# Kernel tuning notes

Hardware: AMD Instinct MI355X
Metric: run time of the kernel (lower is better)

Reference implementation:

```python
import jax, jax.numpy as jnp
import numpy as np

N = 6144       # nodes
E = 12288      # edges (~2N for a sparse simplicial complex)
NF = 32        # node features
EF = 16        # edge features
NH = [32, 32]  # node_hidden
EH = [16, 16]  # edge_hidden
EPS = 1e-5


def setup_inputs() -> dict:
    key = jax.random.key(0)
    ks = jax.random.split(key, 24)
    s = 0.1  # weight init scale
    inp = {}
    inp["X_n"] = jax.random.normal(ks[0], (N, NF), jnp.float32)
    inp["X_e"] = jax.random.normal(ks[1], (E, EF), jnp.float32)
    # normalized adjacency-like operator (non-negative, row mass ~1)
    inp["A_tilde"] = jax.random.uniform(ks[2], (N, N), jnp.float32) * (1.0 / N)
    # normalized Hodge-1 Laplacian-like operator
    inp["L1_tilde"] = jax.random.normal(ks[3], (E, E), jnp.float32) * (1.0 / np.sqrt(E))
    # incidence-like operator
    inp["B1"] = jax.random.normal(ks[4], (N, E), jnp.float32) * (1.0 / np.sqrt(E))
    # GNN linear layers: weight [out, in] (torch convention)
    inp["gnn_W0"] = jax.random.normal(ks[5], (NH[0], NF), jnp.float32) * s
    inp["gnn_b0"] = jnp.zeros((NH[0],), jnp.float32)
    inp["gnn_W1"] = jax.random.normal(ks[6], (NH[1], NH[0]), jnp.float32) * s
    inp["gnn_b1"] = jnp.zeros((NH[1],), jnp.float32)
    # HoSC layer 0: theta in=EF out=EH[0], BN params
    inp["th_W0"] = jax.random.normal(ks[7], (EH[0], EF), jnp.float32) * s
    inp["th_b0"] = jnp.zeros((EH[0],), jnp.float32)
    inp["bn_g0"] = jnp.ones((EH[0],), jnp.float32)
    inp["bn_b0"] = jnp.zeros((EH[0],), jnp.float32)
    # HoSC layer 1: input collapses to 1 channel (max keepdim)
    inp["th_W1"] = jax.random.normal(ks[8], (EH[1], 1), jnp.float32) * s
    inp["th_b1"] = jnp.zeros((EH[1],), jnp.float32)
    inp["bn_g1"] = jnp.ones((EH[1],), jnp.float32)
    inp["bn_b1"] = jnp.zeros((EH[1],), jnp.float32)
    # head: fc1 in = NH[-1] + len(EH) = 34, out = 2N; fc2 out = 1
    inp["fc1_W"] = jax.random.normal(ks[9], (2 * N, NH[-1] + len(EH)), jnp.float32) * s
    inp["fc1_b"] = jnp.zeros((2 * N,), jnp.float32)
    inp["fc2_W"] = jax.random.normal(ks[10], (1, 2 * N), jnp.float32) * s
    inp["fc2_b"] = jnp.zeros((1,), jnp.float32)
    return inp


def _gnn_layer(A, H, W, b):
    # H <- relu((A @ H) @ W^T + b)
    return jax.nn.relu(jnp.matmul(jnp.matmul(A, H), W.T) + b)


def _hosc_layer(Z, L1, W, b, g, beta):
    Zt = jnp.matmul(Z, W.T) + b            # theta
    Zc = jnp.matmul(L1, Zt)                # Laplacian conv
    m = jnp.mean(Zc, axis=0)               # BatchNorm1d (training-mode batch stats)
    v = jnp.var(Zc, axis=0)
    Zp = jax.nn.relu(g * (Zc - m) * jax.lax.rsqrt(v + EPS) + beta)
    return jnp.max(Zp, axis=1, keepdims=True)  # [E, 1]


def reference(X_n, X_e, A_tilde, L1_tilde, B1,
              gnn_W0, gnn_b0, gnn_W1, gnn_b1,
              th_W0, th_b0, bn_g0, bn_b0,
              th_W1, th_b1, bn_g1, bn_b1,
              fc1_W, fc1_b, fc2_W, fc2_b):
    # GNN over nodes
    H = _gnn_layer(A_tilde, X_n, gnn_W0, gnn_b0)
    H_n = _gnn_layer(A_tilde, H, gnn_W1, gnn_b1)      # [N, NH[-1]]
    # HoSC over edges
    Z0 = _hosc_layer(X_e, L1_tilde, th_W0, th_b0, bn_g0, bn_b0)  # [E, 1]
    Z1 = _hosc_layer(Z0, L1_tilde, th_W1, th_b1, bn_g1, bn_b1)   # [E, 1]
    Z_cat = jnp.concatenate([Z0, Z1], axis=1)         # [E, 2]
    H_e = jnp.matmul(B1, Z_cat)                       # [N, 2]
    # head
    Hcat = jnp.concatenate([H_n, H_e], axis=1)        # [N, 34]
    f = jax.nn.relu(jnp.matmul(Hcat, fc1_W.T) + fc1_b)
    f = jnp.matmul(f, fc2_W.T) + fc2_b                # [N, 1]
    return jax.nn.sigmoid(f).squeeze(-1)              # [N]
```

## Files before the change

kernel.cpp:

```cpp
#include <hip/hip_runtime.h>
#include <hip/hip_cooperative_groups.h>
#include <math.h>

namespace cg = cooperative_groups;

#define NND 6144
#define NED 12288
#define GRID 1024
static constexpr float EPS_BN = 1e-5f;

#define HN_OFF    0
#define HE_OFF    196608
#define ST_OFF    208896
#define Y_OFF     208960
#define T0_OFF    405568
#define T1_OFF    602176
#define Z0_OFF    798784
#define Z1_OFF    811072
#define U_OFF     823360
#define S_OFF     835648
#define PP_OFF    847936

typedef float floatx4 __attribute__((ext_vector_type(4)));

__device__ __forceinline__ float4 ntload4(const float* p) {
  floatx4 v = __builtin_nontemporal_load(reinterpret_cast<const floatx4*>(p));
  return make_float4(v.x, v.y, v.z, v.w);
}
__device__ __forceinline__ float4 ld4(const float* p) {
  return *reinterpret_cast<const float4*>(p);
}
__device__ __forceinline__ void gll16(const float* g, float* l) {
  __builtin_amdgcn_global_load_lds(
      (const __attribute__((address_space(1))) unsigned int*)g,
      (__attribute__((address_space(3))) unsigned int*)l, 16, 0, 0);
}

struct Params {
  const float *X_n, *X_e, *A, *L1, *B1;
  const float *gW0, *gb0, *gW1, *gb1;
  const float *tW0, *tb0, *bng0, *bnb0;
  const float *tW1, *tb1, *bng1, *bnb1;
  const float *fc1W, *fc1b, *fc2W, *fc2b;
  float *ws;
  float *out;
};

template<int PHASE>
__global__ __launch_bounds__(256, 4) void pipeline(Params p) {
  __shared__ float lds[10240];
  float* sst = &lds[10176];
  float* red = &lds[10208];

  const int tid  = threadIdx.x;
  const int lane = tid & 63;
  const int w    = tid >> 6;
  const int blk  = blockIdx.x;
  const int gtid = blk * 256 + tid;
  constexpr bool ALL = (PHASE == 0);

  float* Hn = p.ws + HN_OFF;
  float* he = p.ws + HE_OFF;
  float* st = p.ws + ST_OFF;
  float* Y  = p.ws + Y_OFF;
  float* T0 = p.ws + T0_OFF;
  float* T1 = p.ws + T1_OFF;
  float* Z0 = p.ws + Z0_OFF;
  float* Z1 = p.ws + Z1_OFF;
  float* u  = p.ws + U_OFF;
  float* s  = p.ws + S_OFF;
  float* pp = p.ws + PP_OFF;

  auto gemm32 = [&](const float* bias, float* outp) {
    const int rg = w >> 1, cg_ = w & 1;
    const int r0 = blk * 6;
    const int c0 = cg_ * 16;
    float acc[3][16];
    #pragma unroll
    for (int r = 0; r < 3; ++r)
      #pragma unroll
      for (int c = 0; c < 16; ++c) acc[r][c] = 0.f;

    for (int kb = 0; kb < NND; kb += 256) {
      #pragma unroll
      for (int i = 0; i < 8; ++i) {
        const int yr = w * 8 + i;
        gll16(Y + (size_t)yr * NND + kb + lane * 4, &lds[yr * 256]);
      }
      #pragma unroll
      for (int i = 0; i < 2; ++i) {
        const int ar = w * 2 + i;
        if (ar < 6)
          gll16(p.A + (size_t)(r0 + ar) * NND + kb + lane * 4, &lds[8192 + ar * 256]);
      }
      __syncthreads();
      float4 av[3];
      #pragma unroll
      for (int r = 0; r < 3; ++r)
        av[r] = ld4(&lds[8192 + (rg * 3 + r) * 256 + lane * 4]);
      #pragma unroll
      for (int c = 0; c < 16; ++c) {
        const float4 y = ld4(&lds[(c0 + c) * 256 + lane * 4]);
        #pragma unroll
        for (int r = 0; r < 3; ++r) {
          acc[r][c] = fmaf(av[r].x, y.x, acc[r][c]);
          acc[r][c] = fmaf(av[r].y, y.y, acc[r][c]);
          acc[r][c] = fmaf(av[r].z, y.z, acc[r][c]);
          acc[r][c] = fmaf(av[r].w, y.w, acc[r][c]);
        }
      }
      __syncthreads();
    }
    #pragma unroll
    for (int r = 0; r < 3; ++r) {
      float wv[16];
      #pragma unroll
      for (int c = 0; c < 16; ++c) {
        float t = acc[r][c] + __shfl_xor(acc[r][c], 32, 64);
        wv[c] = t + __shfl_xor(t, 16, 64);
      }
      #pragma unroll
      for (int b = 3; b >= 0; --b) {
        const int m = 1 << b;
        const bool hi = (lane & m) != 0;
        #pragma unroll
        for (int i = 0; i < (1 << b); ++i) {
          float x = wv[i], yv = wv[i + (1 << b)];
          float send = hi ? x : yv;
          float recv = __shfl_xor(send, m, 64);
          wv[i] = (hi ? yv : x) + recv;
        }
      }
      if (lane < 16) {
        float v = fmaxf(wv[0] + bias[c0 + lane], 0.f);
        outp[(size_t)(r0 + rg * 3 + r) * 32 + c0 + lane] = v;
      }
    }
  };

  if constexpr (ALL || PHASE == 1) {
    if (blk == 0 && tid < 64) st[tid] = 0.f;
    if (gtid < NND) {
      const int m = gtid;
      float x[32];
      #pragma unroll
      for (int k = 0; k < 32; k += 4) {
        float4 v = ld4(p.X_n + (size_t)m * 32 + k);
        x[k] = v.x; x[k+1] = v.y; x[k+2] = v.z; x[k+3] = v.w;
      }
      #pragma unroll
      for (int oc = 0; oc < 32; ++oc) {
        float acc = 0.f;
        #pragma unroll
        for (int k = 0; k < 32; ++k) acc = fmaf(x[k], p.gW0[oc * 32 + k], acc);
        Y[(size_t)oc * NND + m] = acc;
      }
    } else if (gtid < NND + NED) {
      const int e = gtid - NND;
      float x[16];
      #pragma unroll
      for (int k = 0; k < 16; k += 4) {
        float4 v = ld4(p.X_e + (size_t)e * 16 + k);
        x[k] = v.x; x[k+1] = v.y; x[k+2] = v.z; x[k+3] = v.w;
      }
      #pragma unroll
      for (int oc = 0; oc < 16; ++oc) {
        float acc = p.tb0[oc];
        #pragma unroll
        for (int k = 0; k < 16; ++k) acc = fmaf(x[k], p.tW0[oc * 16 + k], acc);
        T1[(size_t)oc * NED + e] = acc;
      }
    }
  }
  if constexpr (ALL) cg::this_grid().sync();

  if constexpr (ALL || PHASE == 2) gemm32(p.gb0, T0);
  if constexpr (ALL) cg::this_grid().sync();

  if constexpr (ALL || PHASE == 3) {
    if (gtid < NND) {
      const int m = gtid;
      float x[32];
      #pragma unroll
      for (int k = 0; k < 32; k += 4) {
        float4 v = ld4(T0 + (size_t)m * 32 + k);
        x[k] = v.x; x[k+1] = v.y; x[k+2] = v.z; x[k+3] = v.w;
      }
      #pragma unroll
      for (int oc = 0; oc < 32; ++oc) {
        float acc = 0.f;
        #pragma unroll
        for (int k = 0; k < 32; ++k) acc = fmaf(x[k], p.gW1[oc * 32 + k], acc);
        Y[(size_t)oc * NND + m] = acc;
      }
    }
  }
  if constexpr (ALL) cg::this_grid().sync();

  if constexpr (ALL || PHASE == 4) gemm32(p.gb1, Hn);
  if constexpr (ALL) cg::this_grid().sync();

  if constexpr (ALL || PHASE == 5) {
    const int r0 = blk * 12;
    float acc[3][16];
    #pragma unroll
    for (int r = 0; r < 3; ++r)
      #pragma unroll
      for (int c = 0; c < 16; ++c) acc[r][c] = 0.f;

    for (int kb = 0; kb < NED; kb += 256) {
      #pragma unroll
      for (int i = 0; i < 4; ++i) {
        const int yr = w * 4 + i;
        gll16(T1 + (size_t)yr * NED + kb + lane * 4, &lds[yr * 256]);
      }
      #pragma unroll
      for (int i = 0; i < 3; ++i) {
        const int ar = w * 3 + i;
        gll16(p.L1 + (size_t)(r0 + ar) * NED + kb + lane * 4, &lds[4096 + ar * 256]);
      }
      __syncthreads();
      float4 av[3];
      #pragma unroll
      for (int r = 0; r < 3; ++r)
        av[r] = ld4(&lds[4096 + (w * 3 + r) * 256 + lane * 4]);
      #pragma unroll
      for (int c = 0; c < 16; ++c) {
        const float4 y = ld4(&lds[c * 256 + lane * 4]);
        #pragma unroll
        for (int r = 0; r < 3; ++r) {
          acc[r][c] = fmaf(av[r].x, y.x, acc[r][c]);
          acc[r][c] = fmaf(av[r].y, y.y, acc[r][c]);
          acc[r][c] = fmaf(av[r].z, y.z, acc[r][c]);
          acc[r][c] = fmaf(av[r].w, y.w, acc[r][c]);
        }
      }
      __syncthreads();
    }
    float stS = 0.f, stQ = 0.f;
    #pragma unroll
    for (int r = 0; r < 3; ++r) {
      float wv[16];
      #pragma unroll
      for (int c = 0; c < 16; ++c) {
        float t = acc[r][c] + __shfl_xor(acc[r][c], 32, 64);
        wv[c] = t + __shfl_xor(t, 16, 64);
      }
      #pragma unroll
      for (int b = 3; b >= 0; --b) {
        const int m = 1 << b;
        const bool hi = (lane & m) != 0;
        #pragma unroll
        for (int i = 0; i < (1 << b); ++i) {
          float x = wv[i], yv = wv[i + (1 << b)];
          float send = hi ? x : yv;
          float recv = __shfl_xor(send, m, 64);
          wv[i] = (hi ? yv : x) + recv;
        }
      }
      if (lane < 16) {
        const float v = wv[0];
        T0[(size_t)(r0 + w * 3 + r) * 16 + lane] = v;
        stS += v; stQ += v * v;
      }
    }
    if (tid < 32) sst[tid] = 0.f;
    __syncthreads();
    if (lane < 16) {
      atomicAdd(&sst[lane], stS);
      atomicAdd(&sst[16 + lane], stQ);
    }
    __syncthreads();
    if (tid < 32) atomicAdd(st + tid, sst[tid]);
  }
  if constexpr (ALL) cg::this_grid().sync();

  if constexpr (ALL || PHASE == 6) {
    if (gtid < NED) {
      const int e = gtid;
      const float invE = 1.f / (float)NED;
      float best = -3.4e38f;
      #pragma unroll
      for (int c = 0; c < 16; ++c) {
        float m = st[c] * invE;
        float var = st[16 + c] * invE - m * m;
        float sc = p.bng0[c] * rsqrtf(var + EPS_BN);
        float sh = p.bnb0[c] - m * sc;
        best = fmaxf(best, fmaf(T0[(size_t)e * 16 + c], sc, sh));
      }
      Z0[e] = fmaxf(best, 0.f);
    }
  }
  if constexpr (ALL) cg::this_grid().sync();

  if constexpr (ALL || PHASE == 7) {
    const int rb = GRID - 1 - blk;
    const int r0 = rb * 12 + w * 3;
    const float* mp[3];
    #pragma unroll
    for (int r = 0; r < 3; ++r) mp[r] = p.L1 + (size_t)(r0 + r) * NED;
    float ua[3] = {0,0,0}, sa[3] = {0,0,0};
    float4 a[3], an[3];
    #pragma unroll
    for (int r = 0; r < 3; ++r) a[r] = ntload4(mp[r] + lane * 4);
    float4 z = ld4(Z0 + lane * 4), zn;
    for (int kb = 0; kb < NED; kb += 256) {
      const int k = kb + lane * 4;
      const bool more = (kb + 256) < NED;
      if (more) {
        #pragma unroll
        for (int r = 0; r < 3; ++r) an[r] = ntload4(mp[r] + k + 256);
        zn = ld4(Z0 + k + 256);
      }
      #pragma unroll
      for (int r = 0; r < 3; ++r) {
        ua[r] += a[r].x*z.x + a[r].y*z.y + a[r].z*z.z + a[r].w*z.w;
        sa[r] += a[r].x + a[r].y + a[r].z + a[r].w;
      }
      if (more) {
        #pragma unroll
        for (int r = 0; r < 3; ++r) a[r] = an[r];
        z = zn;
      }
    }
    #pragma unroll
    for (int r = 0; r < 3; ++r)
      #pragma unroll
      for (int m = 1; m < 64; m <<= 1) {
        ua[r] += __shfl_xor(ua[r], m, 64);
        sa[r] += __shfl_xor(sa[r], m, 64);
      }
    if (lane == 0) {
      float s1 = 0.f, s2 = 0.f, s3 = 0.f, s4 = 0.f, s5 = 0.f;
      #pragma unroll
      for (int r = 0; r < 3; ++r) {
        u[r0 + r] = ua[r]; s[r0 + r] = sa[r];
        s1 += ua[r]; s2 += sa[r];
        s3 += ua[r] * ua[r]; s4 += sa[r] * sa[r]; s5 += ua[r] * sa[r];
      }
      red[w * 5 + 0] = s1; red[w * 5 + 1] = s2; red[w * 5 + 2] = s3;
      red[w * 5 + 3] = s4; red[w * 5 + 4] = s5;
    }
    __syncthreads();
    if (tid < 5)
      atomicAdd(st + 32 + tid, red[tid] + red[5 + tid] + red[10 + tid] + red[15 + tid]);
  }
  if constexpr (ALL) cg::this_grid().sync();

  if constexpr (ALL || PHASE == 8) {
    if (gtid < NED) {
      const int e = gtid;
      const float invE = 1.f / (float)NED;
      const float Su = st[32], Ss = st[33], Suu = st[34], Sss = st[35], Sus = st[36];
      const float uu = u[e], ssv = s[e];
      float best = -3.4e38f;
      #pragma unroll
      for (int c = 0; c < 16; ++c) {
        const float wc = p.tW1[c], bc = p.tb1[c];
        const float mean = (wc * Su + bc * Ss) * invE;
        const float ex2 = (wc * wc * Suu + 2.f * wc * bc * Sus + bc * bc * Sss) * invE;
        const float var = ex2 - mean * mean;
        const float sc = p.bng1[c] * rsqrtf(var + EPS_BN);
        const float sh = p.bnb1[c] - mean * sc;
        best = fmaxf(best, fmaf(wc * uu + bc * ssv, sc, sh));
      }
      Z1[e] = fmaxf(best, 0.f);
    }
  }
  if constexpr (ALL) cg::this_grid().sync();

  if constexpr (ALL || PHASE == 9) {
    const int r0 = blk * 12 + w * 3;
    if (r0 < NND) {
      const float* mp[3];
      #pragma unroll
      for (int r = 0; r < 3; ++r) mp[r] = p.B1 + (size_t)(r0 + r) * NED;
      float uu[3] = {0,0,0}, vv[3] = {0,0,0};
      float4 a[3], an[3];
      #pragma unroll
      for (int r = 0; r < 3; ++r) a[r] = ntload4(mp[r] + lane * 4);
      float4 z = ld4(Z0 + lane * 4), y = ld4(Z1 + lane * 4), zn, yn;
      for (int kb = 0; kb < NED; kb += 256) {
        const int k = kb + lane * 4;
        const bool more = (kb + 256) < NED;
        if (more) {
          #pragma unroll
          for (int r = 0; r < 3; ++r) an[r] = ntload4(mp[r] + k + 256);
          zn = ld4(Z0 + k + 256); yn = ld4(Z1 + k + 256);
        }
        #pragma unroll
        for (int r = 0; r < 3; ++r) {
          uu[r] += a[r].x*z.x + a[r].y*z.y + a[r].z*z.z + a[r].w*z.w;
          vv[r] += a[r].x*y.x + a[r].y*y.y + a[r].z*y.z + a[r].w*y.w;
        }
        if (more) {
          #pragma unroll
          for (int r = 0; r < 3; ++r) a[r] = an[r];
          z = zn; y = yn;
        }
      }
      #pragma unroll
      for (int r = 0; r < 3; ++r)
        #pragma unroll
        for (int m = 1; m < 64; m <<= 1) {
          uu[r] += __shfl_xor(uu[r], m, 64);
          vv[r] += __shfl_xor(vv[r], m, 64);
        }
      if (lane == 0) {
        #pragma unroll
        for (int r = 0; r < 3; ++r) {
          he[(r0 + r) * 2]     = uu[r];
          he[(r0 + r) * 2 + 1] = vv[r];
        }
      }
    }
  }
  if constexpr (ALL) cg::this_grid().sync();

  if constexpr (ALL || PHASE == 10) {
    const int nb = blk & 7, jb = blk >> 3;
    int n[3];
    float h[3][34];
    float acc[3] = {0.f, 0.f, 0.f};
    #pragma unroll
    for (int i = 0; i < 3; ++i) {
      n[i] = nb * 768 + i * 256 + tid;
      #pragma unroll
      for (int k = 0; k < 32; k += 4) {
        float4 v = ld4(Hn + (size_t)n[i] * 32 + k);
        h[i][k] = v.x; h[i][k+1] = v.y; h[i][k+2] = v.z; h[i][k+3] = v.w;
      }
      float2 e2 = *reinterpret_cast<const float2*>(he + n[i] * 2);
      h[i][32] = e2.x; h[i][33] = e2.y;
    }
    const int j0 = jb * 96;
    for (int j = j0; j < j0 + 96; ++j) {
      const float* wp = p.fc1W + (size_t)j * 34;
      const float bj = p.fc1b[j], vj = p.fc2W[j];
      float s0 = bj, s1 = bj, s2 = bj;
      #pragma unroll
      for (int k = 0; k < 34; ++k) {
        const float wk = wp[k];
        s0 = fmaf(h[0][k], wk, s0);
        s1 = fmaf(h[1][k], wk, s1);
        s2 = fmaf(h[2][k], wk, s2);
      }
      acc[0] += fmaxf(s0, 0.f) * vj;
      acc[1] += fmaxf(s1, 0.f) * vj;
      acc[2] += fmaxf(s2, 0.f) * vj;
    }
    #pragma unroll
    for (int i = 0; i < 3; ++i) pp[(size_t)jb * NND + n[i]] = acc[i];
  }
  if constexpr (ALL) cg::this_grid().sync();

  if constexpr (ALL || PHASE == 11) {
    if (gtid < NND) {
      float acc = 0.f;
      for (int j = 0; j < 128; ++j) acc += pp[(size_t)j * NND + gtid];
      p.out[gtid] = 1.f / (1.f + expf(-(acc + p.fc2b[0])));
    }
  }
}

extern "C" void kernel_launch(void* const* d_in, const int* in_sizes, int n_in,
                              void* d_out, int out_size, void* d_ws, size_t ws_size,
                              hipStream_t stream) {
  Params p;
  p.X_n  = (const float*)d_in[0];
  p.X_e  = (const float*)d_in[1];
  p.A    = (const float*)d_in[2];
  p.L1   = (const float*)d_in[3];
  p.B1   = (const float*)d_in[4];
  p.gW0  = (const float*)d_in[5];
  p.gb0  = (const float*)d_in[6];
  p.gW1  = (const float*)d_in[7];
  p.gb1  = (const float*)d_in[8];
  p.tW0  = (const float*)d_in[9];
  p.tb0  = (const float*)d_in[10];
  p.bng0 = (const float*)d_in[11];
  p.bnb0 = (const float*)d_in[12];
  p.tW1  = (const float*)d_in[13];
  p.tb1  = (const float*)d_in[14];
  p.bng1 = (const float*)d_in[15];
  p.bnb1 = (const float*)d_in[16];
  p.fc1W = (const float*)d_in[17];
  p.fc1b = (const float*)d_in[18];
  p.fc2W = (const float*)d_in[19];
  p.fc2b = (const float*)d_in[20];
  p.ws   = (float*)d_ws;
  p.out  = (float*)d_out;

  int maxBlk = 0;
  hipError_t oe = hipOccupancyMaxActiveBlocksPerMultiprocessor(
      &maxBlk, pipeline<0>, 256, 0);
  bool coop_ok = (oe == hipSuccess) && (maxBlk >= 4);

  if (coop_ok) {
    void* kargs[] = { &p };
    hipError_t le = hipLaunchCooperativeKernel(
        (const void*)&pipeline<0>, dim3(GRID), dim3(256), kargs, 0, stream);
    if (le == hipSuccess) return;
  }

  pipeline<1><<<GRID, 256, 0, stream>>>(p);
  pipeline<2><<<GRID, 256, 0, stream>>>(p);
  pipeline<3><<<GRID, 256, 0, stream>>>(p);
  pipeline<4><<<GRID, 256, 0, stream>>>(p);
  pipeline<5><<<GRID, 256, 0, stream>>>(p);
  pipeline<6><<<GRID, 256, 0, stream>>>(p);
  pipeline<7><<<GRID, 256, 0, stream>>>(p);
  pipeline<8><<<GRID, 256, 0, stream>>>(p);
  pipeline<9><<<GRID, 256, 0, stream>>>(p);
  pipeline<10><<<GRID, 256, 0, stream>>>(p);
  pipeline<11><<<GRID, 256, 0, stream>>>(p);
}
```

Baseline: 578.3 us.

## Double-buffer the second Laplacian GEMM with register prefetch of L1 rows

Phase 5 (L1 times the staged T1 tile) now loads the L1 rows straight into registers and prefetches the next chunk while computing the current one. The T1 tile is double-buffered in LDS through async global-to-LDS loads, and waits use explicit vmcnt counts plus raw s_barrier. This is meant to hide global memory latency behind the FMA loop and drop one barrier per iteration. In exchange it uses more registers and relies on hand-counted vmcnt values, and the launch bounds are rewritten as a waves-per-EU attribute.

```diff
diff --git a/kernel.cpp b/kernel.cpp
--- a/kernel.cpp
+++ b/kernel.cpp
@@ -47,7 +47,9 @@
 };
 
 template<int PHASE>
-__global__ __launch_bounds__(256, 4) void pipeline(Params p) {
+__global__ __launch_bounds__(256)
+__attribute__((amdgpu_waves_per_eu(4, 4)))
+void pipeline(Params p) {
   __shared__ float lds[10240];
   float* sst = &lds[10176];
   float* red = &lds[10208];
@@ -202,41 +204,64 @@
 
   if constexpr (ALL || PHASE == 5) {
     const int r0 = blk * 12;
+    const float* mp[3];
+    #pragma unroll
+    for (int r = 0; r < 3; ++r) mp[r] = p.L1 + (size_t)(r0 + w * 3 + r) * NED;
+
     float acc[3][16];
     #pragma unroll
     for (int r = 0; r < 3; ++r)
       #pragma unroll
       for (int c = 0; c < 16; ++c) acc[r][c] = 0.f;
 
-    for (int kb = 0; kb < NED; kb += 256) {
+    auto stageZt = [&](int kb, int b) {
       #pragma unroll
       for (int i = 0; i < 4; ++i) {
         const int yr = w * 4 + i;
-        gll16(T1 + (size_t)yr * NED + kb + lane * 4, &lds[yr * 256]);
-      }
-      #pragma unroll
-      for (int i = 0; i < 3; ++i) {
-        const int ar = w * 3 + i;
-        gll16(p.L1 + (size_t)(r0 + ar) * NED + kb + lane * 4, &lds[4096 + ar * 256]);
-      }
-      __syncthreads();
-      float4 av[3];
-      #pragma unroll
-      for (int r = 0; r < 3; ++r)
-        av[r] = ld4(&lds[4096 + (w * 3 + r) * 256 + lane * 4]);
+        gll16(T1 + (size_t)yr * NED + kb + lane * 4, &lds[b * 4096 + yr * 256]);
+      }
+    };
+    float4 aC[3], aN[3];
+    auto issueA = [&](int kb, float4* d) {
+      #pragma unroll
+      for (int r = 0; r < 3; ++r) d[r] = ld4(mp[r] + kb + lane * 4);
+    };
+
+    issueA(0, aC);
+    stageZt(0, 0);
+    asm volatile("s_waitcnt vmcnt(0)" ::: "memory");
+    __builtin_amdgcn_sched_barrier(0);
+    __builtin_amdgcn_s_barrier();
+
+    constexpr int NCH = NED / 256;
+    for (int i = 0; i < NCH; ++i) {
+      const int pb = i & 1;
+      const bool more = (i + 1) < NCH;
+      if (more) {
+        issueA((i + 1) * 256, aN);
+        stageZt((i + 1) * 256, pb ^ 1);
+        asm volatile("s_waitcnt vmcnt(7)" ::: "memory");
+      } else {
+        asm volatile("s_waitcnt vmcnt(0)" ::: "memory");
+      }
+      __builtin_amdgcn_sched_barrier(0);
+      __builtin_amdgcn_s_barrier();
+      __builtin_amdgcn_sched_barrier(0);
       #pragma unroll
       for (int c = 0; c < 16; ++c) {
-        const float4 y = ld4(&lds[c * 256 + lane * 4]);
+        const float4 y = ld4(&lds[pb * 4096 + c * 256 + lane * 4]);
         #pragma unroll
         for (int r = 0; r < 3; ++r) {
-          acc[r][c] = fmaf(av[r].x, y.x, acc[r][c]);
-          acc[r][c] = fmaf(av[r].y, y.y, acc[r][c]);
-          acc[r][c] = fmaf(av[r].z, y.z, acc[r][c]);
-          acc[r][c] = fmaf(av[r].w, y.w, acc[r][c]);
-        }
-      }
-      __syncthreads();
-    }
+          acc[r][c] = fmaf(aC[r].x, y.x, acc[r][c]);
+          acc[r][c] = fmaf(aC[r].y, y.y, acc[r][c]);
+          acc[r][c] = fmaf(aC[r].z, y.z, acc[r][c]);
+          acc[r][c] = fmaf(aC[r].w, y.w, acc[r][c]);
+        }
+      }
+      if (more) { aC[0] = aN[0]; aC[1] = aN[1]; aC[2] = aN[2]; }
+      __builtin_amdgcn_s_barrier();
+    }
+
     float stS = 0.f, stQ = 0.f;
     #pragma unroll
     for (int r = 0; r < 3; ++r) {
```

After: 592.7 us. 2.5% more time.

## Merge independent GNN and HoSC phases to cut grid barriers

Applied to the files above, without the earlier changes.

Interleaves the node-GNN stages with the edge-HoSC stages, which do not depend on each other, so each grid-synchronised phase does both a GNN step and a Laplacian step. This drops the phase count from eleven to eight, and with it the number of cooperative grid syncs or fallback launches. The head is re-tiled to one node per thread over 768 blocks with 384 hidden units each, and the final reduction now sums 32 partials instead of 128. Launch bounds change to a waves_per_eu attribute. Merged phases become longer and less balanced, and the head leaves some blocks idle.

```diff
diff --git a/kernel.cpp b/kernel.cpp
--- a/kernel.cpp
+++ b/kernel.cpp
@@ -14,12 +14,13 @@
 #define ST_OFF    208896
 #define Y_OFF     208960
 #define T0_OFF    405568
-#define T1_OFF    602176
-#define Z0_OFF    798784
-#define Z1_OFF    811072
-#define U_OFF     823360
-#define S_OFF     835648
-#define PP_OFF    847936
+#define ZT_OFF    602176
+#define ZC_OFF    798784
+#define Z0_OFF    995392
+#define Z1_OFF    1007680
+#define U_OFF     1019968
+#define S_OFF     1032256
+#define PP_OFF    1044544
 
 typedef float floatx4 __attribute__((ext_vector_type(4)));
 
@@ -47,7 +48,9 @@
 };
 
 template<int PHASE>
-__global__ __launch_bounds__(256, 4) void pipeline(Params p) {
+__global__ __launch_bounds__(256)
+__attribute__((amdgpu_waves_per_eu(4, 4)))
+void pipeline(Params p) {
   __shared__ float lds[10240];
   float* sst = &lds[10176];
   float* red = &lds[10208];
@@ -64,7 +67,8 @@
   float* st = p.ws + ST_OFF;
   float* Y  = p.ws + Y_OFF;
   float* T0 = p.ws + T0_OFF;
-  float* T1 = p.ws + T1_OFF;
+  float* ZT = p.ws + ZT_OFF;
+  float* ZC = p.ws + ZC_OFF;
   float* Z0 = p.ws + Z0_OFF;
   float* Z1 = p.ws + Z1_OFF;
   float* u  = p.ws + U_OFF;
@@ -168,39 +172,15 @@
         float acc = p.tb0[oc];
         #pragma unroll
         for (int k = 0; k < 16; ++k) acc = fmaf(x[k], p.tW0[oc * 16 + k], acc);
-        T1[(size_t)oc * NED + e] = acc;
-      }
-    }
-  }
-  if constexpr (ALL) cg::this_grid().sync();
-
-  if constexpr (ALL || PHASE == 2) gemm32(p.gb0, T0);
-  if constexpr (ALL) cg::this_grid().sync();
-
-  if constexpr (ALL || PHASE == 3) {
-    if (gtid < NND) {
-      const int m = gtid;
-      float x[32];
-      #pragma unroll
-      for (int k = 0; k < 32; k += 4) {
-        float4 v = ld4(T0 + (size_t)m * 32 + k);
-        x[k] = v.x; x[k+1] = v.y; x[k+2] = v.z; x[k+3] = v.w;
-      }
-      #pragma unroll
-      for (int oc = 0; oc < 32; ++oc) {
-        float acc = 0.f;
-        #pragma unroll
-        for (int k = 0; k < 32; ++k) acc = fmaf(x[k], p.gW1[oc * 32 + k], acc);
-        Y[(size_t)oc * NND + m] = acc;
-      }
-    }
-  }
-  if constexpr (ALL) cg::this_grid().sync();
-
-  if constexpr (ALL || PHASE == 4) gemm32(p.gb1, Hn);
-  if constexpr (ALL) cg::this_grid().sync();
-
-  if constexpr (ALL || PHASE == 5) {
+        ZT[(size_t)oc * NED + e] = acc;
+      }
+    }
+  }
+  if constexpr (ALL) cg::this_grid().sync();
+
+  if constexpr (ALL || PHASE == 2) {
+    gemm32(p.gb0, T0);
+
     const int r0 = blk * 12;
     float acc[3][16];
     #pragma unroll
@@ -212,7 +192,7 @@
       #pragma unroll
       for (int i = 0; i < 4; ++i) {
         const int yr = w * 4 + i;
-        gll16(T1 + (size_t)yr * NED + kb + lane * 4, &lds[yr * 256]);
+        gll16(ZT + (size_t)yr * NED + kb + lane * 4, &lds[yr * 256]);
       }
       #pragma unroll
       for (int i = 0; i < 3; ++i) {
@@ -260,7 +240,7 @@
       }
       if (lane < 16) {
         const float v = wv[0];
-        T0[(size_t)(r0 + w * 3 + r) * 16 + lane] = v;
+        ZC[(size_t)(r0 + w * 3 + r) * 16 + lane] = v;
         stS += v; stQ += v * v;
       }
     }
@@ -275,9 +255,24 @@
   }
   if constexpr (ALL) cg::this_grid().sync();
 
-  if constexpr (ALL || PHASE == 6) {
-    if (gtid < NED) {
-      const int e = gtid;
+  if constexpr (ALL || PHASE == 3) {
+    if (gtid < NND) {
+      const int m = gtid;
+      float x[32];
+      #pragma unroll
+      for (int k = 0; k < 32; k += 4) {
+        float4 v = ld4(T0 + (size_t)m * 32 + k);
+        x[k] = v.x; x[k+1] = v.y; x[k+2] = v.z; x[k+3] = v.w;
+      }
+      #pragma unroll
+      for (int oc = 0; oc < 32; ++oc) {
+        float acc = 0.f;
+        #pragma unroll
+        for (int k = 0; k < 32; ++k) acc = fmaf(x[k], p.gW1[oc * 32 + k], acc);
+        Y[(size_t)oc * NND + m] = acc;
+      }
+    } else if (gtid < NND + NED) {
+      const int e = gtid - NND;
       const float invE = 1.f / (float)NED;
       float best = -3.4e38f;
       #pragma unroll
@@ -286,14 +281,16 @@
         float var = st[16 + c] * invE - m * m;
         float sc = p.bng0[c] * rsqrtf(var + EPS_BN);
         float sh = p.bnb0[c] - m * sc;
-        best = fmaxf(best, fmaf(T0[(size_t)e * 16 + c], sc, sh));
+        best = fmaxf(best, fmaf(ZC[(size_t)e * 16 + c], sc, sh));
       }
       Z0[e] = fmaxf(best, 0.f);
     }
   }
   if constexpr (ALL) cg::this_grid().sync();
 
-  if constexpr (ALL || PHASE == 7) {
+  if constexpr (ALL || PHASE == 4) {
+    gemm32(p.gb1, Hn);
+
     const int rb = GRID - 1 - blk;
     const int r0 = rb * 12 + w * 3;
     const float* mp[3];
@@ -347,7 +344,7 @@
   }
   if constexpr (ALL) cg::this_grid().sync();
 
-  if constexpr (ALL || PHASE == 8) {
+  if constexpr (ALL || PHASE == 5) {
     if (gtid < NED) {
       const int e = gtid;
       const float invE = 1.f / (float)NED;
@@ -369,7 +366,7 @@
   }
   if constexpr (ALL) cg::this_grid().sync();
 
-  if constexpr (ALL || PHASE == 9) {
+  if constexpr (ALL || PHASE == 6) {
     const int r0 = blk * 12 + w * 3;
     if (r0 < NND) {
       const float* mp[3];
@@ -417,47 +414,37 @@
   }
   if constexpr (ALL) cg::this_grid().sync();
 
-  if constexpr (ALL || PHASE == 10) {
-    const int nb = blk & 7, jb = blk >> 3;
-    int n[3];
-    float h[3][34];
-    float acc[3] = {0.f, 0.f, 0.f};
-    #pragma unroll
-    for (int i = 0; i < 3; ++i) {
-      n[i] = nb * 768 + i * 256 + tid;
+  if constexpr (ALL || PHASE == 7) {
+    if (blk < 768) {
+      const int nb = blk % 24, jb = blk / 24;
+      const int n = nb * 256 + tid;
+      float h[34];
       #pragma unroll
       for (int k = 0; k < 32; k += 4) {
-        float4 v = ld4(Hn + (size_t)n[i] * 32 + k);
-        h[i][k] = v.x; h[i][k+1] = v.y; h[i][k+2] = v.z; h[i][k+3] = v.w;
-      }
-      float2 e2 = *reinterpret_cast<const float2*>(he + n[i] * 2);
-      h[i][32] = e2.x; h[i][33] = e2.y;
-    }
-    const int j0 = jb * 96;
-    for (int j = j0; j < j0 + 96; ++j) {
-      const float* wp = p.fc1W + (size_t)j * 34;
-      const float bj = p.fc1b[j], vj = p.fc2W[j];
-      float s0 = bj, s1 = bj, s2 = bj;
-      #pragma unroll
-      for (int k = 0; k < 34; ++k) {
-        const float wk = wp[k];
-        s0 = fmaf(h[0][k], wk, s0);
-        s1 = fmaf(h[1][k], wk, s1);
-        s2 = fmaf(h[2][k], wk, s2);
-      }
-      acc[0] += fmaxf(s0, 0.f) * vj;
-      acc[1] += fmaxf(s1, 0.f) * vj;
-      acc[2] += fmaxf(s2, 0.f) * vj;
-    }
-    #pragma unroll
-    for (int i = 0; i < 3; ++i) pp[(size_t)jb * NND + n[i]] = acc[i];
-  }
-  if constexpr (ALL) cg::this_grid().sync();
-
-  if constexpr (ALL || PHASE == 11) {
+        float4 v = ld4(Hn + (size_t)n * 32 + k);
+        h[k] = v.x; h[k+1] = v.y; h[k+2] = v.z; h[k+3] = v.w;
+      }
+      float2 e2 = *reinterpret_cast<const float2*>(he + n * 2);
+      h[32] = e2.x; h[33] = e2.y;
+      float acc = 0.f;
+      const int j0 = jb * 384;
+      for (int j = j0; j < j0 + 384; ++j) {
+        const float* wp = p.fc1W + (size_t)j * 34;
+        float s0 = p.fc1b[j];
+        #pragma unroll
+        for (int k = 0; k < 34; ++k) s0 = fmaf(h[k], wp[k], s0);
+        acc = fmaf(fmaxf(s0, 0.f), p.fc2W[j], acc);
+      }
+      pp[(size_t)jb * NND + n] = acc;
+    }
+  }
+  if constexpr (ALL) cg::this_grid().sync();
+
+  if constexpr (ALL || PHASE == 8) {
     if (gtid < NND) {
       float acc = 0.f;
-      for (int j = 0; j < 128; ++j) acc += pp[(size_t)j * NND + gtid];
+      #pragma unroll
+      for (int j = 0; j < 32; ++j) acc += pp[(size_t)j * NND + gtid];
       p.out[gtid] = 1.f / (1.f + expf(-(acc + p.fc2b[0])));
     }
   }
@@ -511,7 +498,4 @@
   pipeline<6><<<GRID, 256, 0, stream>>>(p);
   pipeline<7><<<GRID, 256, 0, stream>>>(p);
   pipeline<8><<<GRID, 256, 0, stream>>>(p);
-  pipeline<9><<<GRID, 256, 0, stream>>>(p);
-  pipeline<10><<<GRID, 256, 0, stream>>>(p);
-  pipeline<11><<<GRID, 256, 0, stream>>>(p);
 }
```

Measured after the change: 711.2 us. 23.0% more time.

## Stream L1/B1 matvecs through LDS rings and split head into separate kernels

Applied to the files above, without the earlier changes.

The L1 matvec phase and the B1 projection phase now stage matrix rows and the Z vectors into per-wave LDS ring buffers with global_load_lds, using explicit vmcnt waits for a multi-stage software pipeline. Before, they used register double-buffered nontemporal loads. Phase 9 now runs on only the even blocks. The fc1/fc2 head and the final reduction move out of the cooperative kernel into two standalone kernels with a different grid shape, each head block covering 192 outputs, which removes two grid-wide syncs. The workspace is re-laid out so the conv output and the transposed features get separate buffers. The hand-written waitcnt sequencing is fragile, and the extra launches add some overhead.

```diff
diff --git a/kernel.cpp b/kernel.cpp
--- a/kernel.cpp
+++ b/kernel.cpp
@@ -14,19 +14,16 @@
 #define ST_OFF    208896
 #define Y_OFF     208960
 #define T0_OFF    405568
-#define T1_OFF    602176
-#define Z0_OFF    798784
-#define Z1_OFF    811072
-#define U_OFF     823360
-#define S_OFF     835648
-#define PP_OFF    847936
+#define ZC_OFF    602176
+#define ZT_OFF    798784
+#define Z0_OFF    995392
+#define Z1_OFF    1007680
+#define U_OFF     1019968
+#define S_OFF     1032256
+#define PP_OFF    1044544
 
 typedef float floatx4 __attribute__((ext_vector_type(4)));
 
-__device__ __forceinline__ float4 ntload4(const float* p) {
-  floatx4 v = __builtin_nontemporal_load(reinterpret_cast<const floatx4*>(p));
-  return make_float4(v.x, v.y, v.z, v.w);
-}
 __device__ __forceinline__ float4 ld4(const float* p) {
   return *reinterpret_cast<const float4*>(p);
 }
@@ -47,7 +44,8 @@
 };
 
 template<int PHASE>
-__global__ __launch_bounds__(256, 4) void pipeline(Params p) {
+__global__ __launch_bounds__(256, 4)
+void pipeline(Params p) {
   __shared__ float lds[10240];
   float* sst = &lds[10176];
   float* red = &lds[10208];
@@ -64,12 +62,12 @@
   float* st = p.ws + ST_OFF;
   float* Y  = p.ws + Y_OFF;
   float* T0 = p.ws + T0_OFF;
-  float* T1 = p.ws + T1_OFF;
+  float* ZC = p.ws + ZC_OFF;
+  float* ZT = p.ws + ZT_OFF;
   float* Z0 = p.ws + Z0_OFF;
   float* Z1 = p.ws + Z1_OFF;
   float* u  = p.ws + U_OFF;
   float* s  = p.ws + S_OFF;
-  float* pp = p.ws + PP_OFF;
 
   auto gemm32 = [&](const float* bias, float* outp) {
     const int rg = w >> 1, cg_ = w & 1;
@@ -168,7 +166,7 @@
         float acc = p.tb0[oc];
         #pragma unroll
         for (int k = 0; k < 16; ++k) acc = fmaf(x[k], p.tW0[oc * 16 + k], acc);
-        T1[(size_t)oc * NED + e] = acc;
+        ZT[(size_t)oc * NED + e] = acc;
       }
     }
   }
@@ -212,7 +210,7 @@
       #pragma unroll
       for (int i = 0; i < 4; ++i) {
         const int yr = w * 4 + i;
-        gll16(T1 + (size_t)yr * NED + kb + lane * 4, &lds[yr * 256]);
+        gll16(ZT + (size_t)yr * NED + kb + lane * 4, &lds[yr * 256]);
       }
       #pragma unroll
       for (int i = 0; i < 3; ++i) {
@@ -260,7 +258,7 @@
       }
       if (lane < 16) {
         const float v = wv[0];
-        T0[(size_t)(r0 + w * 3 + r) * 16 + lane] = v;
+        ZC[(size_t)(r0 + w * 3 + r) * 16 + lane] = v;
         stS += v; stQ += v * v;
       }
     }
@@ -286,7 +284,7 @@
         float var = st[16 + c] * invE - m * m;
         float sc = p.bng0[c] * rsqrtf(var + EPS_BN);
         float sh = p.bnb0[c] - m * sc;
-        best = fmaxf(best, fmaf(T0[(size_t)e * 16 + c], sc, sh));
+        best = fmaxf(best, fmaf(ZC[(size_t)e * 16 + c], sc, sh));
       }
       Z0[e] = fmaxf(best, 0.f);
     }
@@ -296,50 +294,47 @@
   if constexpr (ALL || PHASE == 7) {
     const int rb = GRID - 1 - blk;
     const int r0 = rb * 12 + w * 3;
-    const float* mp[3];
-    #pragma unroll
-    for (int r = 0; r < 3; ++r) mp[r] = p.L1 + (size_t)(r0 + r) * NED;
-    float ua[3] = {0,0,0}, sa[3] = {0,0,0};
-    float4 a[3], an[3];
-    #pragma unroll
-    for (int r = 0; r < 3; ++r) a[r] = ntload4(mp[r] + lane * 4);
-    float4 z = ld4(Z0 + lane * 4), zn;
-    for (int kb = 0; kb < NED; kb += 256) {
-      const int k = kb + lane * 4;
-      const bool more = (kb + 256) < NED;
-      if (more) {
-        #pragma unroll
-        for (int r = 0; r < 3; ++r) an[r] = ntload4(mp[r] + k + 256);
-        zn = ld4(Z0 + k + 256);
-      }
-      #pragma unroll
-      for (int r = 0; r < 3; ++r) {
-        ua[r] += a[r].x*z.x + a[r].y*z.y + a[r].z*z.z + a[r].w*z.w;
-        sa[r] += a[r].x + a[r].y + a[r].z + a[r].w;
-      }
-      if (more) {
-        #pragma unroll
-        for (int r = 0; r < 3; ++r) a[r] = an[r];
-        z = zn;
-      }
-    }
-    #pragma unroll
-    for (int r = 0; r < 3; ++r)
+    float* aring = &lds[w * 2048];
+    float* zring = &lds[w * 2048 + 1024];
+    float us5[5] = {0.f, 0.f, 0.f, 0.f, 0.f};
+    for (int r = 0; r < 3; ++r) {
+      const float* mp = p.L1 + (size_t)(r0 + r) * NED;
+      float ua = 0.f, sa = 0.f;
+      #pragma unroll
+      for (int d = 0; d < 4; ++d) {
+        gll16(mp + d * 256 + lane * 4, aring + d * 256);
+        gll16(Z0 + d * 256 + lane * 4, zring + d * 256);
+      }
+      for (int i = 0; i < 48; ++i) {
+        if (i <= 44)      asm volatile("s_waitcnt vmcnt(6)" ::: "memory");
+        else if (i == 45) asm volatile("s_waitcnt vmcnt(4)" ::: "memory");
+        else if (i == 46) asm volatile("s_waitcnt vmcnt(2)" ::: "memory");
+        else              asm volatile("s_waitcnt vmcnt(0)" ::: "memory");
+        __builtin_amdgcn_sched_barrier(0);
+        const int s_ = i & 3;
+        float4 a = ld4(aring + s_ * 256 + lane * 4);
+        float4 z = ld4(zring + s_ * 256 + lane * 4);
+        ua += a.x*z.x + a.y*z.y + a.z*z.z + a.w*z.w;
+        sa += a.x + a.y + a.z + a.w;
+        if (i < 44) {
+          asm volatile("s_waitcnt lgkmcnt(0)" ::: "memory");
+          __builtin_amdgcn_sched_barrier(0);
+          gll16(mp + (i + 4) * 256 + lane * 4, aring + s_ * 256);
+          gll16(Z0 + (i + 4) * 256 + lane * 4, zring + s_ * 256);
+        }
+      }
       #pragma unroll
       for (int m = 1; m < 64; m <<= 1) {
-        ua[r] += __shfl_xor(ua[r], m, 64);
-        sa[r] += __shfl_xor(sa[r], m, 64);
-      }
+        ua += __shfl_xor(ua, m, 64);
+        sa += __shfl_xor(sa, m, 64);
+      }
+      if (lane == 0) { u[r0 + r] = ua; s[r0 + r] = sa; }
+      us5[0] += ua; us5[1] += sa;
+      us5[2] += ua * ua; us5[3] += sa * sa; us5[4] += ua * sa;
+    }
     if (lane == 0) {
-      float s1 = 0.f, s2 = 0.f, s3 = 0.f, s4 = 0.f, s5 = 0.f;
-      #pragma unroll
-      for (int r = 0; r < 3; ++r) {
-        u[r0 + r] = ua[r]; s[r0 + r] = sa[r];
-        s1 += ua[r]; s2 += sa[r];
-        s3 += ua[r] * ua[r]; s4 += sa[r] * sa[r]; s5 += ua[r] * sa[r];
-      }
-      red[w * 5 + 0] = s1; red[w * 5 + 1] = s2; red[w * 5 + 2] = s3;
-      red[w * 5 + 3] = s4; red[w * 5 + 4] = s5;
+      #pragma unroll
+      for (int q = 0; q < 5; ++q) red[w * 5 + q] = us5[q];
     }
     __syncthreads();
     if (tid < 5)
@@ -370,97 +365,103 @@
   if constexpr (ALL) cg::this_grid().sync();
 
   if constexpr (ALL || PHASE == 9) {
-    const int r0 = blk * 12 + w * 3;
-    if (r0 < NND) {
-      const float* mp[3];
-      #pragma unroll
-      for (int r = 0; r < 3; ++r) mp[r] = p.B1 + (size_t)(r0 + r) * NED;
-      float uu[3] = {0,0,0}, vv[3] = {0,0,0};
-      float4 a[3], an[3];
-      #pragma unroll
-      for (int r = 0; r < 3; ++r) a[r] = ntload4(mp[r] + lane * 4);
-      float4 z = ld4(Z0 + lane * 4), y = ld4(Z1 + lane * 4), zn, yn;
-      for (int kb = 0; kb < NED; kb += 256) {
-        const int k = kb + lane * 4;
-        const bool more = (kb + 256) < NED;
-        if (more) {
-          #pragma unroll
-          for (int r = 0; r < 3; ++r) an[r] = ntload4(mp[r] + k + 256);
-          zn = ld4(Z0 + k + 256); yn = ld4(Z1 + k + 256);
-        }
-        #pragma unroll
-        for (int r = 0; r < 3; ++r) {
-          uu[r] += a[r].x*z.x + a[r].y*z.y + a[r].z*z.z + a[r].w*z.w;
-          vv[r] += a[r].x*y.x + a[r].y*y.y + a[r].z*y.z + a[r].w*y.w;
-        }
-        if (more) {
-          #pragma unroll
-          for (int r = 0; r < 3; ++r) a[r] = an[r];
-          z = zn; y = yn;
-        }
-      }
-      #pragma unroll
-      for (int r = 0; r < 3; ++r)
+    if ((blk & 1) == 0) {
+      const int r0 = (blk >> 1) * 12 + w * 3;
+      float* aring = &lds[w * 2304];
+      float* zring = &lds[w * 2304 + 768];
+      float* yring = &lds[w * 2304 + 1536];
+      for (int r = 0; r < 3; ++r) {
+        const float* mp = p.B1 + (size_t)(r0 + r) * NED;
+        float uu = 0.f, vv = 0.f;
+        #pragma unroll
+        for (int d = 0; d < 3; ++d) {
+          gll16(mp + d * 256 + lane * 4, aring + d * 256);
+          gll16(Z0 + d * 256 + lane * 4, zring + d * 256);
+          gll16(Z1 + d * 256 + lane * 4, yring + d * 256);
+        }
+        int s_ = 0;
+        for (int i = 0; i < 48; ++i) {
+          if (i <= 45)      asm volatile("s_waitcnt vmcnt(6)" ::: "memory");
+          else if (i == 46) asm volatile("s_waitcnt vmcnt(3)" ::: "memory");
+          else              asm volatile("s_waitcnt vmcnt(0)" ::: "memory");
+          __builtin_amdgcn_sched_barrier(0);
+          float4 a = ld4(aring + s_ * 256 + lane * 4);
+          float4 z = ld4(zring + s_ * 256 + lane * 4);
+          float4 y = ld4(yring + s_ * 256 + lane * 4);
+          uu += a.x*z.x + a.y*z.y + a.z*z.z + a.w*z.w;
+          vv += a.x*y.x + a.y*y.y + a.z*y.z + a.w*y.w;
+          if (i < 45) {
+            asm volatile("s_waitcnt lgkmcnt(0)" ::: "memory");
+            __builtin_amdgcn_sched_barrier(0);
+            gll16(mp + (i + 3) * 256 + lane * 4, aring + s_ * 256);
+            gll16(Z0 + (i + 3) * 256 + lane * 4, zring + s_ * 256);
+            gll16(Z1 + (i + 3) * 256 + lane * 4, yring + s_ * 256);
+          }
+          s_ = (s_ == 2) ? 0 : s_ + 1;
+        }
         #pragma unroll
         for (int m = 1; m < 64; m <<= 1) {
-          uu[r] += __shfl_xor(uu[r], m, 64);
-          vv[r] += __shfl_xor(vv[r], m, 64);
-        }
-      if (lane == 0) {
-        #pragma unroll
-        for (int r = 0; r < 3; ++r) {
-          he[(r0 + r) * 2]     = uu[r];
-          he[(r0 + r) * 2 + 1] = vv[r];
-        }
-      }
-    }
-  }
-  if constexpr (ALL) cg::this_grid().sync();
-
-  if constexpr (ALL || PHASE == 10) {
-    const int nb = blk & 7, jb = blk >> 3;
-    int n[3];
-    float h[3][34];
-    float acc[3] = {0.f, 0.f, 0.f};
+          uu += __shfl_xor(uu, m, 64);
+          vv += __shfl_xor(vv, m, 64);
+        }
+        if (lane == 0) {
+          he[(r0 + r) * 2]     = uu;
+          he[(r0 + r) * 2 + 1] = vv;
+        }
+      }
+    }
+  }
+}
+
+__global__ __launch_bounds__(256, 2)
+void k10_head(const float* __restrict__ Hn, const float* __restrict__ he,
+              const float* __restrict__ W1, const float* __restrict__ b1,
+              const float* __restrict__ w2, float* __restrict__ pp) {
+  const int t = threadIdx.x;
+  const int nb = blockIdx.x;
+  const int jb = blockIdx.y;
+  int n[3];
+  float h[3][34];
+  float acc[3] = {0.f, 0.f, 0.f};
+  #pragma unroll
+  for (int i = 0; i < 3; ++i) {
+    n[i] = nb * 768 + i * 256 + t;
     #pragma unroll
-    for (int i = 0; i < 3; ++i) {
-      n[i] = nb * 768 + i * 256 + tid;
-      #pragma unroll
-      for (int k = 0; k < 32; k += 4) {
-        float4 v = ld4(Hn + (size_t)n[i] * 32 + k);
-        h[i][k] = v.x; h[i][k+1] = v.y; h[i][k+2] = v.z; h[i][k+3] = v.w;
-      }
-      float2 e2 = *reinterpret_cast<const float2*>(he + n[i] * 2);
-      h[i][32] = e2.x; h[i][33] = e2.y;
-    }
-    const int j0 = jb * 96;
-    for (int j = j0; j < j0 + 96; ++j) {
-      const float* wp = p.fc1W + (size_t)j * 34;
-      const float bj = p.fc1b[j], vj = p.fc2W[j];
-      float s0 = bj, s1 = bj, s2 = bj;
-      #pragma unroll
-      for (int k = 0; k < 34; ++k) {
-        const float wk = wp[k];
-        s0 = fmaf(h[0][k], wk, s0);
-        s1 = fmaf(h[1][k], wk, s1);
-        s2 = fmaf(h[2][k], wk, s2);
-      }
-      acc[0] += fmaxf(s0, 0.f) * vj;
-      acc[1] += fmaxf(s1, 0.f) * vj;
-      acc[2] += fmaxf(s2, 0.f) * vj;
-    }
+    for (int k = 0; k < 32; k += 4) {
+      float4 v = ld4(Hn + (size_t)n[i] * 32 + k);
+      h[i][k] = v.x; h[i][k+1] = v.y; h[i][k+2] = v.z; h[i][k+3] = v.w;
+    }
+    float2 e2 = *reinterpret_cast<const float2*>(he + n[i] * 2);
+    h[i][32] = e2.x; h[i][33] = e2.y;
+  }
+  const int j0 = jb * 192;
+  for (int j = j0; j < j0 + 192; ++j) {
+    const float* wp = W1 + (size_t)j * 34;
+    const float bj = b1[j], vj = w2[j];
+    float s0 = bj, s1 = bj, s2 = bj;
     #pragma unroll
-    for (int i = 0; i < 3; ++i) pp[(size_t)jb * NND + n[i]] = acc[i];
-  }
-  if constexpr (ALL) cg::this_grid().sync();
-
-  if constexpr (ALL || PHASE == 11) {
-    if (gtid < NND) {
-      float acc = 0.f;
-      for (int j = 0; j < 128; ++j) acc += pp[(size_t)j * NND + gtid];
-      p.out[gtid] = 1.f / (1.f + expf(-(acc + p.fc2b[0])));
-    }
-  }
+    for (int k = 0; k < 34; ++k) {
+      const float wk = wp[k];
+      s0 = fmaf(h[0][k], wk, s0);
+      s1 = fmaf(h[1][k], wk, s1);
+      s2 = fmaf(h[2][k], wk, s2);
+    }
+    acc[0] += fmaxf(s0, 0.f) * vj;
+    acc[1] += fmaxf(s1, 0.f) * vj;
+    acc[2] += fmaxf(s2, 0.f) * vj;
+  }
+  #pragma unroll
+  for (int i = 0; i < 3; ++i) pp[(size_t)jb * NND + n[i]] = acc[i];
+}
+
+__global__ __launch_bounds__(256)
+void k11_final(const float* __restrict__ pp, const float* __restrict__ b2,
+               float* __restrict__ out) {
+  const int i = blockIdx.x * 256 + threadIdx.x;
+  float acc = 0.f;
+  #pragma unroll
+  for (int j = 0; j < 64; ++j) acc += pp[(size_t)j * NND + i];
+  out[i] = 1.f / (1.f + expf(-(acc + b2[0])));
 }
 
 extern "C" void kernel_launch(void* const* d_in, const int* in_sizes, int n_in,
@@ -491,27 +492,34 @@
   p.ws   = (float*)d_ws;
   p.out  = (float*)d_out;
 
+  float* ws = (float*)d_ws;
+  float* pp = ws + PP_OFF;
+
   int maxBlk = 0;
   hipError_t oe = hipOccupancyMaxActiveBlocksPerMultiprocessor(
       &maxBlk, pipeline<0>, 256, 0);
   bool coop_ok = (oe == hipSuccess) && (maxBlk >= 4);
 
+  bool launched = false;
   if (coop_ok) {
     void* kargs[] = { &p };
     hipError_t le = hipLaunchCooperativeKernel(
         (const void*)&pipeline<0>, dim3(GRID), dim3(256), kargs, 0, stream);
-    if (le == hipSuccess) return;
-  }
-
-  pipeline<1><<<GRID, 256, 0, stream>>>(p);
-  pipeline<2><<<GRID, 256, 0, stream>>>(p);
-  pipeline<3><<<GRID, 256, 0, stream>>>(p);
-  pipeline<4><<<GRID, 256, 0, stream>>>(p);
-  pipeline<5><<<GRID, 256, 0, stream>>>(p);
-  pipeline<6><<<GRID, 256, 0, stream>>>(p);
-  pipeline<7><<<GRID, 256, 0, stream>>>(p);
-  pipeline<8><<<GRID, 256, 0, stream>>>(p);
-  pipeline<9><<<GRID, 256, 0, stream>>>(p);
-  pipeline<10><<<GRID, 256, 0, stream>>>(p);
-  pipeline<11><<<GRID, 256, 0, stream>>>(p);
+    launched = (le == hipSuccess);
+  }
+  if (!launched) {
+    pipeline<1><<<GRID, 256, 0, stream>>>(p);
+    pipeline<2><<<GRID, 256, 0, stream>>>(p);
+    pipeline<3><<<GRID, 256, 0, stream>>>(p);
+    pipeline<4><<<GRID, 256, 0, stream>>>(p);
+    pipeline<5><<<GRID, 256, 0, stream>>>(p);
+    pipeline<6><<<GRID, 256, 0, stream>>>(p);
+    pipeline<7><<<GRID, 256, 0, stream>>>(p);
+    pipeline<8><<<GRID, 256, 0, stream>>>(p);
+    pipeline<9><<<GRID, 256, 0, stream>>>(p);
+  }
+
+  k10_head<<<dim3(8, 64), 256, 0, stream>>>(p.ws + HN_OFF, p.ws + HE_OFF,
+                                            p.fc1W, p.fc1b, p.fc2W, pp);
+  k11_final<<<24, 256, 0, stream>>>(pp, p.fc2b, p.out);
 }
```

New measurement: 705.3 us. 1.22x slower.
